# Optimization experiments

Hardware: AMD Instinct MI355X
Metric: run time of the kernel (lower is better)

Reference implementation:

```python
import jax, jax.numpy as jnp
import numpy as np

EMBED_DIM = 2048
NUM_HEADS = 32
NUM_KV_HEADS = 8
HEAD_DIM = EMBED_DIM // NUM_HEADS  # 64
KV_DIM = NUM_KV_HEADS * HEAD_DIM   # 512


def setup_inputs() -> dict:
    key = jax.random.key(0)
    ks = jax.random.split(key, 5)
    B, S = 2, 2048
    scale = 0.02
    x = jax.random.normal(ks[0], (B, S, EMBED_DIM), dtype=jnp.float32)
    Wq = jax.random.normal(ks[1], (EMBED_DIM, EMBED_DIM), dtype=jnp.float32) * scale
    Wk = jax.random.normal(ks[2], (EMBED_DIM, KV_DIM), dtype=jnp.float32) * scale
    Wv = jax.random.normal(ks[3], (EMBED_DIM, KV_DIM), dtype=jnp.float32) * scale
    Wo = jax.random.normal(ks[4], (EMBED_DIM, EMBED_DIM), dtype=jnp.float32) * scale
    return {"x": x, "Wq": Wq, "Wk": Wk, "Wv": Wv, "Wo": Wo}


def reference(x, Wq, Wk, Wv, Wo):
    B, S, _ = x.shape
    g = NUM_HEADS // NUM_KV_HEADS  # queries per kv head
    # projections -> [B, H, S, D]
    q = (x @ Wq).reshape(B, S, NUM_HEADS, HEAD_DIM).transpose(0, 2, 1, 3)
    k = (x @ Wk).reshape(B, S, NUM_KV_HEADS, HEAD_DIM).transpose(0, 2, 1, 3)
    v = (x @ Wv).reshape(B, S, NUM_KV_HEADS, HEAD_DIM).transpose(0, 2, 1, 3)
    # GQA repeat_interleave on head dim
    k = jnp.repeat(k, g, axis=1)
    v = jnp.repeat(v, g, axis=1)
    scores = jnp.einsum('bhqd,bhkd->bhqk', q, k) / np.sqrt(HEAD_DIM).astype(np.float32)
    causal = jnp.tril(jnp.ones((S, S), dtype=bool))
    scores = jnp.where(causal, scores, jnp.finfo(x.dtype).min)
    attn = jax.nn.softmax(scores, axis=-1)
    out = jnp.einsum('bhqk,bhkd->bhqd', attn, v)  # [B, H, S, D]
    out = out.transpose(0, 2, 1, 3).reshape(B, S, EMBED_DIM)
    return out @ Wo
```

## Files before the change

kernel.cpp:

```cpp
#include <hip/hip_runtime.h>
#include <hip/hip_bf16.h>
#include <cstdint>
#include <type_traits>

#define EMBED 2048
#define SLEN 2048
#define NB 2
#define NHEADS 32
#define HDIM 64
#define KVDIM 512
#define MTOT (NB * SLEN)
#define NQKV (EMBED + 2 * KVDIM)

typedef __attribute__((ext_vector_type(8))) __bf16 bf16x8;
typedef __attribute__((ext_vector_type(4))) float f32x4;
typedef __attribute__((ext_vector_type(16))) float f32x16;

#define QSCALE 0.18033688011112042f

__device__ __forceinline__ ushort f2bf(float f) {
    union { float f; uint32_t u; } v; v.f = f;
    uint32_t r = (v.u + 0x7FFFu + ((v.u >> 16) & 1u)) >> 16;
    return (ushort)r;
}

__device__ __forceinline__ void gload_lds16(const ushort* g, ushort* l) {
    __builtin_amdgcn_global_load_lds(
        (const __attribute__((address_space(1))) void*)g,
        (__attribute__((address_space(3))) void*)l, 16, 0, 0);
}

__global__ __launch_bounds__(256) void k_prep(const float* __restrict__ x,
                                              const float* __restrict__ Wq,
                                              const float* __restrict__ Wk,
                                              const float* __restrict__ Wv,
                                              const float* __restrict__ Wo,
                                              ushort* __restrict__ xb,
                                              ushort* __restrict__ wt,
                                              ushort* __restrict__ wot) {
    const int tid = threadIdx.x;
    int bid = blockIdx.x;
    if (bid < 8192) {
        int i = bid * 256 + tid;
        float4 v = *(const float4*)(x + (size_t)i * 4);
        ushort4 o;
        o.x = f2bf(v.x); o.y = f2bf(v.y); o.z = f2bf(v.z); o.w = f2bf(v.w);
        *(ushort4*)(xb + (size_t)i * 4) = o;
        return;
    }
    bid -= 8192;
    const float* W; ushort* Wt; int N; float scale; int bx, by;
    if (bid < 4096)      { W = Wq; Wt = wt;                                   N = EMBED; scale = QSCALE; bx = bid & 63; by = bid >> 6; }
    else if (bid < 5120) { W = Wk; Wt = wt + (size_t)EMBED * EMBED;           N = KVDIM; scale = 1.f; int b2 = bid - 4096; bx = b2 & 15; by = b2 >> 4; }
    else if (bid < 6144) { W = Wv; Wt = wt + (size_t)(EMBED + KVDIM) * EMBED; N = KVDIM; scale = 1.f; int b2 = bid - 5120; bx = b2 & 15; by = b2 >> 4; }
    else                 { W = Wo; Wt = wot;                                  N = EMBED; scale = 1.f; int b2 = bid - 6144; bx = b2 & 63; by = b2 >> 6; }
    const int K = EMBED;
    __shared__ float tile[32][33];
    const int tx = tid & 31, ty = tid >> 5;
    const int xcol = bx * 32 + tx;
    const int y0 = by * 32;
    #pragma unroll
    for (int i = ty; i < 32; i += 8)
        tile[i][tx] = W[(size_t)(y0 + i) * N + xcol];
    __syncthreads();
    const int xo = y0 + tx;
    const int yo0 = bx * 32;
    #pragma unroll
    for (int i = ty; i < 32; i += 8)
        Wt[(size_t)(yo0 + i) * K + xo] = f2bf(tile[tx][i] * scale);
}

__global__ __launch_bounds__(256) void k_transpose_v(const ushort* __restrict__ V,
                                                     ushort* __restrict__ VT) {
    __shared__ ushort tile[64][65];
    const int tx = threadIdx.x, ty = threadIdx.y;
    const int x0 = blockIdx.x * 64;
    const int y0 = blockIdx.y * 64;
    #pragma unroll
    for (int i = ty; i < 64; i += 4)
        tile[i][tx] = V[(size_t)(y0 + i) * KVDIM + x0 + tx];
    __syncthreads();
    #pragma unroll
    for (int i = ty; i < 64; i += 4)
        VT[(size_t)(x0 + i) * MTOT + y0 + tx] = tile[tx][i];
}

__global__ __launch_bounds__(256) void k_gemm_qkv(const ushort* __restrict__ A,
                                                  const ushort* __restrict__ Bt,
                                                  ushort* __restrict__ Qb,
                                                  ushort* __restrict__ Kb,
                                                  ushort* __restrict__ Vb) {
    __shared__ alignas(16) ushort As[128 * 32];
    __shared__ alignas(16) ushort Bs[128 * 32];

    const int tid = threadIdx.x;
    const int lane = tid & 63;
    const int w = tid >> 6;
    const int wr = w >> 1, wc = w & 1;
    const int l15 = lane & 15, g = lane >> 4;
    const int m0 = blockIdx.y * 128;
    const int n0 = blockIdx.x * 128;
    const int K = EMBED;

    f32x4 acc[4][4] = {};

    const int c0 = tid, c1 = tid + 256;
    const int rA0 = c0 >> 2, sA0 = c0 & 3;
    const int rA1 = c1 >> 2, sA1 = c1 & 3;

    const ushort* pA0 = A + (size_t)(m0 + rA0) * K + sA0 * 8;
    const ushort* pA1 = A + (size_t)(m0 + rA1) * K + sA1 * 8;
    const ushort* pB0 = Bt + (size_t)(n0 + rA0) * K + sA0 * 8;
    const ushort* pB1 = Bt + (size_t)(n0 + rA1) * K + sA1 * 8;

    for (int k0 = 0; k0 < K; k0 += 32) {
        __syncthreads();
        gload_lds16(pA0 + k0, As + c0 * 8);
        gload_lds16(pA1 + k0, As + c1 * 8);
        gload_lds16(pB0 + k0, Bs + c0 * 8);
        gload_lds16(pB1 + k0, Bs + c1 * 8);
        __syncthreads();

        bf16x8 a[4], b[4];
        #pragma unroll
        for (int i = 0; i < 4; i++)
            a[i] = *(const bf16x8*)&As[(wr * 64 + i * 16 + l15) * 32 + 8 * g];
        #pragma unroll
        for (int j = 0; j < 4; j++)
            b[j] = *(const bf16x8*)&Bs[(wc * 64 + j * 16 + l15) * 32 + 8 * g];
        #pragma unroll
        for (int i = 0; i < 4; i++)
            #pragma unroll
            for (int j = 0; j < 4; j++)
                acc[i][j] = __builtin_amdgcn_mfma_f32_16x16x32_bf16(a[i], b[j], acc[i][j], 0, 0, 0);
    }

    ushort* Cb; int Nout, cbase;
    if (n0 < EMBED)              { Cb = Qb; Nout = EMBED; cbase = n0; }
    else if (n0 < EMBED + KVDIM) { Cb = Kb; Nout = KVDIM; cbase = n0 - EMBED; }
    else                         { Cb = Vb; Nout = KVDIM; cbase = n0 - EMBED - KVDIM; }

    #pragma unroll
    for (int i = 0; i < 4; i++) {
        #pragma unroll
        for (int j = 0; j < 4; j++) {
            const int row = m0 + wr * 64 + i * 16 + g * 4;
            const int col = cbase + wc * 64 + j * 16 + l15;
            #pragma unroll
            for (int r = 0; r < 4; r++)
                Cb[(size_t)(row + r) * Nout + col] = f2bf(acc[i][j][r]);
        }
    }
}

template <typename OUT_T>
__global__ __launch_bounds__(256) void k_gemm_bt(const ushort* __restrict__ A,
                                                 const ushort* __restrict__ Bt,
                                                 OUT_T* __restrict__ C,
                                                 int M, int N, int K) {
    __shared__ alignas(16) ushort As[128 * 64];
    __shared__ alignas(16) ushort Bs[128 * 64];

    const int tid = threadIdx.x;
    const int lane = tid & 63;
    const int w = tid >> 6;
    const int wr = w >> 1, wc = w & 1;
    const int l15 = lane & 15, g = lane >> 4;
    const int m0 = blockIdx.y * 128;
    const int n0 = blockIdx.x * 128;

    f32x4 acc[4][4] = {};

    const ushort* pA[4];
    const ushort* pB[4];
    #pragma unroll
    for (int t = 0; t < 4; t++) {
        const int c = tid + 256 * t;
        const int r = c >> 3, gr = c & 7;
        const int sg = gr ^ (r & 7);
        pA[t] = A + (size_t)(m0 + r) * K + sg * 8;
        pB[t] = Bt + (size_t)(n0 + r) * K + sg * 8;
    }

    for (int k0 = 0; k0 < K; k0 += 64) {
        __syncthreads();
        #pragma unroll
        for (int t = 0; t < 4; t++) {
            gload_lds16(pA[t] + k0, As + (tid + 256 * t) * 8);
            gload_lds16(pB[t] + k0, Bs + (tid + 256 * t) * 8);
        }
        __syncthreads();

        #pragma unroll
        for (int kk = 0; kk < 2; kk++) {
            bf16x8 a[4], b[4];
            #pragma unroll
            for (int i = 0; i < 4; i++)
                a[i] = *(const bf16x8*)&As[(wr * 64 + i * 16 + l15) * 64 +
                                           (((4 * kk + g) ^ (l15 & 7)) << 3)];
            #pragma unroll
            for (int j = 0; j < 4; j++)
                b[j] = *(const bf16x8*)&Bs[(wc * 64 + j * 16 + l15) * 64 +
                                           (((4 * kk + g) ^ (l15 & 7)) << 3)];
            #pragma unroll
            for (int i = 0; i < 4; i++)
                #pragma unroll
                for (int j = 0; j < 4; j++)
                    acc[i][j] = __builtin_amdgcn_mfma_f32_16x16x32_bf16(a[i], b[j], acc[i][j], 0, 0, 0);
        }
    }

    #pragma unroll
    for (int i = 0; i < 4; i++) {
        #pragma unroll
        for (int j = 0; j < 4; j++) {
            const int row = m0 + wr * 64 + i * 16 + g * 4;
            const int col = n0 + wc * 64 + j * 16 + l15;
            #pragma unroll
            for (int r = 0; r < 4; r++) {
                float val = acc[i][j][r];
                if constexpr (std::is_same<OUT_T, ushort>::value)
                    C[(size_t)(row + r) * N + col] = f2bf(val);
                else
                    C[(size_t)(row + r) * N + col] = val;
            }
        }
    }
}

__global__ __launch_bounds__(512, 4) void k_attn(const ushort* __restrict__ Qg,
                                                 const ushort* __restrict__ Kg,
                                                 const ushort* __restrict__ VTg,
                                                 ushort* __restrict__ Og) {
    __shared__ alignas(16) ushort Ks[2][64 * 64];
    __shared__ alignas(16) ushort Vs[2][64 * 64];

    const int tid = threadIdx.x;
    const int lane = tid & 63;
    const int wq = tid >> 6;
    const int l31 = lane & 31;
    const int hi = lane >> 5;

    const int flat = blockIdx.x + (blockIdx.y << 3) + (blockIdx.z << 8);
    const int lo = flat & 255, hv = flat >> 8;
    const int bi = hv ? (7 - (lo & 7)) : (lo & 7);
    const int h = lo >> 3;
    const int b = hv;
    const int kh = h >> 2;
    const size_t rowbase = (size_t)b * SLEN;

    const int q0 = bi * 256;
    const int qw0 = q0 + wq * 32;
    const int nt = (q0 >> 6) + 4;

    bf16x8 qf[4];
    {
        const ushort* qrow = Qg + (rowbase + qw0 + l31) * EMBED + h * HDIM;
        #pragma unroll
        for (int s = 0; s < 4; s++)
            qf[s] = *(const bf16x8*)(qrow + s * 16 + hi * 8);
    }

    const int srow = tid >> 3;
    const int sgr = tid & 7;
    const int woff = srow * 64 + ((sgr ^ (srow & 7)) << 3);
    const ushort* kgbase = Kg + (rowbase + srow) * KVDIM + kh * HDIM + sgr * 8;
    const ushort* vgbase = VTg + (size_t)(kh * HDIM + srow) * MTOT + b * SLEN + sgr * 8;

    {
        uint4 kr = *(const uint4*)kgbase;
        uint4 vr = *(const uint4*)vgbase;
        *(uint4*)&Ks[0][woff] = kr;
        *(uint4*)&Vs[0][woff] = vr;
    }
    __syncthreads();

    f32x16 oacc[2];
    #pragma unroll
    for (int d = 0; d < 2; d++)
        #pragma unroll
        for (int r = 0; r < 16; r++) oacc[d][r] = 0.f;
    float l_run = 0.f;

    int cur = 0;
    for (int kt = 0; kt < nt; ++kt) {
        const int k0 = kt * 64;
        const bool pref = (kt + 1 < nt);
        uint4 kr, vr;
        if (pref) {
            kr = *(const uint4*)(kgbase + (size_t)(k0 + 64) * KVDIM);
            vr = *(const uint4*)(vgbase + k0 + 64);
        }

        if (k0 <= qw0 + 31) {
            f32x16 sacc[2];
            #pragma unroll
            for (int st = 0; st < 2; st++)
                #pragma unroll
                for (int r = 0; r < 16; r++) sacc[st][r] = 0.f;
            __builtin_amdgcn_s_setprio(1);
            #pragma unroll
            for (int st = 0; st < 2; st++) {
                const int krow = st * 32 + l31;
                #pragma unroll
                for (int s = 0; s < 4; s++) {
                    bf16x8 af = *(const bf16x8*)&Ks[cur][krow * 64 + (((2 * s + hi) ^ (l31 & 7)) << 3)];
                    sacc[st] = __builtin_amdgcn_mfma_f32_32x32x16_bf16(af, qf[s], sacc[st], 0, 0, 0);
                }
            }
            __builtin_amdgcn_s_setprio(0);
            if (k0 + 63 > qw0) {
                const int q = qw0 + l31;
                #pragma unroll
                for (int st = 0; st < 2; st++)
                    #pragma unroll
                    for (int r = 0; r < 16; r++) {
                        int kpos = k0 + st * 32 + (r & 3) + 8 * (r >> 2) + 4 * hi;
                        if (kpos > q) sacc[st][r] = -1e30f;
                    }
            }
            float lsum = 0.f;
            #pragma unroll
            for (int st = 0; st < 2; st++)
                #pragma unroll
                for (int r = 0; r < 16; r++) {
                    float p = __builtin_amdgcn_exp2f(sacc[st][r]);
                    sacc[st][r] = p;
                    lsum += p;
                }
            lsum += __shfl_xor(lsum, 32);
            l_run += lsum;
            uint32_t pr[2][8];
            #pragma unroll
            for (int st = 0; st < 2; st++)
                #pragma unroll
                for (int k = 0; k < 8; k++) {
                    uint32_t d;
                    asm("v_cvt_pk_bf16_f32 %0, %1, %2"
                        : "=v"(d) : "v"(sacc[st][2 * k]), "v"(sacc[st][2 * k + 1]));
                    pr[st][k] = d;
                }
            #pragma unroll
            for (int c = 0; c < 2; c++) {
                #pragma unroll
                for (int tt = 0; tt < 2; tt++) {
                    const int pb = 4 * tt;
                    uint32_t w0 = pr[c][pb + 0], w2 = pr[c][pb + 2];
                    uint32_t w1 = pr[c][pb + 1], w3 = pr[c][pb + 3];
                    asm("v_permlane32_swap_b32 %0, %1" : "+v"(w0), "+v"(w2));
                    asm("v_permlane32_swap_b32 %0, %1" : "+v"(w1), "+v"(w3));
                    union { uint32_t u[4]; bf16x8 v; } pf;
                    pf.u[0] = w0; pf.u[1] = w1; pf.u[2] = w2; pf.u[3] = w3;
                    const int t = 2 * c + tt;
                    __builtin_amdgcn_s_setprio(1);
                    #pragma unroll
                    for (int dt = 0; dt < 2; dt++) {
                        const int vrow = dt * 32 + l31;
                        bf16x8 vf = *(const bf16x8*)&Vs[cur][vrow * 64 + (((2 * t + hi) ^ (l31 & 7)) << 3)];
                        oacc[dt] = __builtin_amdgcn_mfma_f32_32x32x16_bf16(pf.v, vf, oacc[dt], 0, 0, 0);
                    }
                    __builtin_amdgcn_s_setprio(0);
                }
            }
        }

        __syncthreads();
        if (pref) {
            *(uint4*)&Ks[cur ^ 1][woff] = kr;
            *(uint4*)&Vs[cur ^ 1][woff] = vr;
        }
        __syncthreads();
        cur ^= 1;
    }

    #pragma unroll
    for (int r = 0; r < 16; r++) {
        const int rr = (r & 3) + 8 * (r >> 2) + 4 * hi;
        float lr = __shfl(l_run, rr | (lane & 32));
        float inv = 1.f / lr;
        const size_t base = (rowbase + qw0 + rr) * EMBED + h * HDIM;
        Og[base + l31] = f2bf(oacc[0][r] * inv);
        Og[base + 32 + l31] = f2bf(oacc[1][r] * inv);
    }
}

#define WS_XB  ((size_t)0)
#define WS_QB  (WS_XB + (size_t)MTOT * EMBED)
#define WS_KB  (WS_QB + (size_t)MTOT * EMBED)
#define WS_VB  (WS_KB + (size_t)MTOT * KVDIM)
#define WS_WT  (WS_VB + (size_t)MTOT * KVDIM)
#define WS_WOT (WS_WT + (size_t)NQKV * EMBED)
#define WS_VT  WS_WT

extern "C" void kernel_launch(void* const* d_in, const int* in_sizes, int n_in,
                              void* d_out, int out_size, void* d_ws, size_t ws_size,
                              hipStream_t stream) {
    const float* x  = (const float*)d_in[0];
    const float* Wq = (const float*)d_in[1];
    const float* Wk = (const float*)d_in[2];
    const float* Wv = (const float*)d_in[3];
    const float* Wo = (const float*)d_in[4];
    float* out = (float*)d_out;
    ushort* ws = (ushort*)d_ws;

    k_prep<<<18432, 256, 0, stream>>>(x, Wq, Wk, Wv, Wo,
                                      ws + WS_XB, ws + WS_WT, ws + WS_WOT);

    k_gemm_qkv<<<dim3(NQKV / 128, MTOT / 128), 256, 0, stream>>>(
        ws + WS_XB, ws + WS_WT, ws + WS_QB, ws + WS_KB, ws + WS_VB);

    k_transpose_v<<<dim3(KVDIM / 64, MTOT / 64), dim3(64, 4), 0, stream>>>(
        ws + WS_VB, ws + WS_VT);

    k_attn<<<dim3(8, 32, 2), 512, 0, stream>>>(
        ws + WS_QB, ws + WS_KB, ws + WS_VT, ws + WS_XB);

    k_gemm_bt<float><<<dim3(EMBED / 128, MTOT / 128), 256, 0, stream>>>(
        ws + WS_XB, ws + WS_WOT, out, MTOT, EMBED, EMBED);
}
```

Baseline: 192.1 us.

## Double-buffer LDS tiles and add XCD-aware block swizzle in GEMM kernels

Both GEMM kernels now keep two LDS buffers and prefetch the next K-slice while MFMAs consume the current one. This removes one barrier per iteration and hides global-to-LDS latency. Block indices are also remapped so consecutive tiles land on the same XCD, which is meant to improve L2 reuse. The cost is doubled LDS use per block, which may lower occupancy, and correctness relies on the grid size being a multiple of 8.

```diff
diff --git a/kernel.cpp b/kernel.cpp
--- a/kernel.cpp
+++ b/kernel.cpp
@@ -85,21 +85,30 @@
         VT[(size_t)(x0 + i) * MTOT + y0 + tx] = tile[tx][i];
 }
 
+__device__ __forceinline__ int2 xcd_swizzle(int gx, int gy) {
+    const int nwg = gx * gy;
+    int f = blockIdx.y * gx + blockIdx.x;
+    const int cpx = nwg >> 3;
+    f = (f & 7) * cpx + (f >> 3);
+    return make_int2(f % gx, f / gx);
+}
+
 __global__ __launch_bounds__(256) void k_gemm_qkv(const ushort* __restrict__ A,
                                                   const ushort* __restrict__ Bt,
                                                   ushort* __restrict__ Qb,
                                                   ushort* __restrict__ Kb,
                                                   ushort* __restrict__ Vb) {
-    __shared__ alignas(16) ushort As[128 * 32];
-    __shared__ alignas(16) ushort Bs[128 * 32];
+    __shared__ alignas(16) ushort As[2][128 * 32];
+    __shared__ alignas(16) ushort Bs[2][128 * 32];
 
     const int tid = threadIdx.x;
     const int lane = tid & 63;
     const int w = tid >> 6;
     const int wr = w >> 1, wc = w & 1;
     const int l15 = lane & 15, g = lane >> 4;
-    const int m0 = blockIdx.y * 128;
-    const int n0 = blockIdx.x * 128;
+    const int2 bxy = xcd_swizzle(NQKV / 128, MTOT / 128);
+    const int n0 = bxy.x * 128;
+    const int m0 = bxy.y * 128;
     const int K = EMBED;
 
     f32x4 acc[4][4] = {};
@@ -113,26 +122,34 @@
     const ushort* pB0 = Bt + (size_t)(n0 + rA0) * K + sA0 * 8;
     const ushort* pB1 = Bt + (size_t)(n0 + rA1) * K + sA1 * 8;
 
+    gload_lds16(pA0, &As[0][c0 * 8]);
+    gload_lds16(pA1, &As[0][c1 * 8]);
+    gload_lds16(pB0, &Bs[0][c0 * 8]);
+    gload_lds16(pB1, &Bs[0][c1 * 8]);
+    __syncthreads();
+
+    int cur = 0;
     for (int k0 = 0; k0 < K; k0 += 32) {
-        __syncthreads();
-        gload_lds16(pA0 + k0, As + c0 * 8);
-        gload_lds16(pA1 + k0, As + c1 * 8);
-        gload_lds16(pB0 + k0, Bs + c0 * 8);
-        gload_lds16(pB1 + k0, Bs + c1 * 8);
-        __syncthreads();
-
+        if (k0 + 32 < K) {
+            gload_lds16(pA0 + k0 + 32, &As[cur ^ 1][c0 * 8]);
+            gload_lds16(pA1 + k0 + 32, &As[cur ^ 1][c1 * 8]);
+            gload_lds16(pB0 + k0 + 32, &Bs[cur ^ 1][c0 * 8]);
+            gload_lds16(pB1 + k0 + 32, &Bs[cur ^ 1][c1 * 8]);
+        }
         bf16x8 a[4], b[4];
         #pragma unroll
         for (int i = 0; i < 4; i++)
-            a[i] = *(const bf16x8*)&As[(wr * 64 + i * 16 + l15) * 32 + 8 * g];
+            a[i] = *(const bf16x8*)&As[cur][(wr * 64 + i * 16 + l15) * 32 + 8 * g];
         #pragma unroll
         for (int j = 0; j < 4; j++)
-            b[j] = *(const bf16x8*)&Bs[(wc * 64 + j * 16 + l15) * 32 + 8 * g];
+            b[j] = *(const bf16x8*)&Bs[cur][(wc * 64 + j * 16 + l15) * 32 + 8 * g];
         #pragma unroll
         for (int i = 0; i < 4; i++)
             #pragma unroll
             for (int j = 0; j < 4; j++)
                 acc[i][j] = __builtin_amdgcn_mfma_f32_16x16x32_bf16(a[i], b[j], acc[i][j], 0, 0, 0);
+        __syncthreads();
+        cur ^= 1;
     }
 
     ushort* Cb; int Nout, cbase;
@@ -158,16 +175,17 @@
                                                  const ushort* __restrict__ Bt,
                                                  OUT_T* __restrict__ C,
                                                  int M, int N, int K) {
-    __shared__ alignas(16) ushort As[128 * 64];
-    __shared__ alignas(16) ushort Bs[128 * 64];
+    __shared__ alignas(16) ushort As[2][128 * 64];
+    __shared__ alignas(16) ushort Bs[2][128 * 64];
 
     const int tid = threadIdx.x;
     const int lane = tid & 63;
     const int w = tid >> 6;
     const int wr = w >> 1, wc = w & 1;
     const int l15 = lane & 15, g = lane >> 4;
-    const int m0 = blockIdx.y * 128;
-    const int n0 = blockIdx.x * 128;
+    const int2 bxy = xcd_swizzle(N / 128, M / 128);
+    const int n0 = bxy.x * 128;
+    const int m0 = bxy.y * 128;
 
     f32x4 acc[4][4] = {};
 
@@ -182,32 +200,41 @@
         pB[t] = Bt + (size_t)(n0 + r) * K + sg * 8;
     }
 
+    #pragma unroll
+    for (int t = 0; t < 4; t++) {
+        gload_lds16(pA[t], &As[0][(tid + 256 * t) * 8]);
+        gload_lds16(pB[t], &Bs[0][(tid + 256 * t) * 8]);
+    }
+    __syncthreads();
+
+    int cur = 0;
     for (int k0 = 0; k0 < K; k0 += 64) {
-        __syncthreads();
-        #pragma unroll
-        for (int t = 0; t < 4; t++) {
-            gload_lds16(pA[t] + k0, As + (tid + 256 * t) * 8);
-            gload_lds16(pB[t] + k0, Bs + (tid + 256 * t) * 8);
-        }
-        __syncthreads();
-
+        if (k0 + 64 < K) {
+            #pragma unroll
+            for (int t = 0; t < 4; t++) {
+                gload_lds16(pA[t] + k0 + 64, &As[cur ^ 1][(tid + 256 * t) * 8]);
+                gload_lds16(pB[t] + k0 + 64, &Bs[cur ^ 1][(tid + 256 * t) * 8]);
+            }
+        }
         #pragma unroll
         for (int kk = 0; kk < 2; kk++) {
             bf16x8 a[4], b[4];
             #pragma unroll
             for (int i = 0; i < 4; i++)
-                a[i] = *(const bf16x8*)&As[(wr * 64 + i * 16 + l15) * 64 +
-                                           (((4 * kk + g) ^ (l15 & 7)) << 3)];
+                a[i] = *(const bf16x8*)&As[cur][(wr * 64 + i * 16 + l15) * 64 +
+                                                (((4 * kk + g) ^ (l15 & 7)) << 3)];
             #pragma unroll
             for (int j = 0; j < 4; j++)
-                b[j] = *(const bf16x8*)&Bs[(wc * 64 + j * 16 + l15) * 64 +
-                                           (((4 * kk + g) ^ (l15 & 7)) << 3)];
+                b[j] = *(const bf16x8*)&Bs[cur][(wc * 64 + j * 16 + l15) * 64 +
+                                                (((4 * kk + g) ^ (l15 & 7)) << 3)];
             #pragma unroll
             for (int i = 0; i < 4; i++)
                 #pragma unroll
                 for (int j = 0; j < 4; j++)
                     acc[i][j] = __builtin_amdgcn_mfma_f32_16x16x32_bf16(a[i], b[j], acc[i][j], 0, 0, 0);
         }
+        __syncthreads();
+        cur ^= 1;
     }
 
     #pragma unroll
```

Result: no change. 189.4 us (-1.4%).
